# Kernel optimization log

Measured on AMD Instinct MI355X. Metric: run time of the kernel, lower is better.

The kernel has to match this reference:

```python
import jax, jax.numpy as jnp
import numpy as np


def sign_fn(x):
    # torch.sign(torch.sign(x) + 0.5): maps x >= 0 -> +1, x < 0 -> -1 (zero -> +1)
    return jnp.where(x >= 0, 1.0, -1.0).astype(x.dtype)


def setup_inputs() -> dict:
    key = jax.random.key(0)
    kx, kw, kb = jax.random.split(key, 3)
    TOKENS, IN, OUT = 8192, 4096, 4096
    x = jax.random.normal(kx, (TOKENS, IN), dtype=jnp.float32)
    weight = jax.random.normal(kw, (OUT, IN), dtype=jnp.float32)
    bias = jax.random.normal(kb, (OUT,), dtype=jnp.float32)
    return {"x": x, "weight": weight, "bias": bias}


def reference(x, weight, bias):
    b_weight = sign_fn(weight)  # [out, in], values in {+1, -1}
    b_bias = sign_fn(bias)      # [out]
    # nn.functional.linear: y = x @ W^T + b
    return jnp.einsum('ti,oi->to', x, b_weight) + b_bias
```

## Files before the change

### kernel.cpp

```cpp
#include <hip/hip_runtime.h>


typedef __attribute__((ext_vector_type(4))) int   i32x4;
typedef __attribute__((ext_vector_type(8))) short short8;
typedef __attribute__((ext_vector_type(4))) float f32x4;

constexpr int M = 8192;
constexpr int N = 4096;
constexpr int K = 4096;

constexpr int BM = 256, BN = 256, BK = 64;
constexpr int NTILES = K / BK;
constexpr int TILE_A = BM * BK;
constexpr int TILE_B = BN * BK;
constexpr int BUFSZ  = TILE_A + TILE_B;
constexpr int RING   = 4;

__device__ __forceinline__ void load_lds16(const void* g, void* l) {
    __builtin_amdgcn_global_load_lds(
        (const __attribute__((address_space(1))) unsigned int*)g,
        (__attribute__((address_space(3))) unsigned int*)l, 16, 0, 0);
}

constexpr int XB = M / 4;
constexpr int WB = 1024;
constexpr int WCH = N * K / 8;

__global__ __launch_bounds__(256) void prep_fused(
    const float* __restrict__ X, const float* __restrict__ W,
    signed char* __restrict__ Xq, signed char* __restrict__ Wq,
    float* __restrict__ Scale) {
    const int t    = threadIdx.x;
    const int lane = t & 63;
    const int wv   = t >> 6;

    if (blockIdx.x < XB) {
        const int row = blockIdx.x * 4 + wv;
        const float4* xr = reinterpret_cast<const float4*>(X + (size_t)row * K);
        float4 v[16];
        float mx = 0.f;
#pragma unroll
        for (int i = 0; i < 4; ++i) {
#pragma unroll
            for (int j = 0; j < 4; ++j) {
                float4 f = xr[4 * lane + 256 * i + j];
                v[4 * i + j] = f;
                mx = fmaxf(mx, fmaxf(fmaxf(fabsf(f.x), fabsf(f.y)),
                                     fmaxf(fabsf(f.z), fabsf(f.w))));
            }
        }
#pragma unroll
        for (int off = 32; off > 0; off >>= 1)
            mx = fmaxf(mx, __shfl_down(mx, off));
        mx = __shfl(mx, 0);
        const float rmax = fmaxf(mx, 1e-20f);
        const float inv  = 127.f / rmax;
        if (lane == 0) Scale[row] = rmax * (1.f / 127.f);

        uint4* out4 = reinterpret_cast<uint4*>(Xq + (size_t)row * K);
#pragma unroll
        for (int i = 0; i < 4; ++i) {
            uint4 o;
            unsigned int* op = &o.x;
#pragma unroll
            for (int j = 0; j < 4; ++j) {
                float4 f = v[4 * i + j];
                int q0 = (int)rintf(f.x * inv);
                int q1 = (int)rintf(f.y * inv);
                int q2 = (int)rintf(f.z * inv);
                int q3 = (int)rintf(f.w * inv);
                op[j] = (q0 & 255) | ((q1 & 255) << 8) |
                        ((q2 & 255) << 16) | ((unsigned)(q3 & 255) << 24);
            }
            out4[lane + 64 * i] = o;
        }
    } else {
        const float4* W4 = reinterpret_cast<const float4*>(W);
        uint2* O = reinterpret_cast<uint2*>(Wq);
        auto sg = [](float f) -> unsigned int { return (f >= 0.f) ? 1u : 0xFFu; };
        size_t idx = (size_t)(blockIdx.x - XB) * 256 + t;
        const size_t stride = (size_t)WB * 256;
        for (size_t c = idx; c < (size_t)WCH; c += stride) {
            float4 a = W4[c * 2], b = W4[c * 2 + 1];
            uint2 o;
            o.x = sg(a.x) | (sg(a.y) << 8) | (sg(a.z) << 16) | (sg(a.w) << 24);
            o.y = sg(b.x) | (sg(b.y) << 8) | (sg(b.z) << 16) | (sg(b.w) << 24);
            O[c] = o;
        }
    }
}

struct GemmCtx {
    const signed char* gA0;
    const signed char* gA1;
    const signed char* gB0;
    const signed char* gB1;
    signed char* lbase;
    int wm, wn, rl, cq16;
};

template <int P, bool STAGE>
__device__ __forceinline__ void phase(
    const GemmCtx& c, const signed char* Ab, const signed char* Bb,
    signed char* dst, size_t ko,
    i32x4 (&a)[2], i32x4 (&b)[4], i32x4 (&acc)[8][4]) {
    if constexpr (P == 0) {
#pragma unroll
        for (int ni = 0; ni < 4; ++ni)
            b[ni] = *reinterpret_cast<const i32x4*>(
                Bb + (c.wn * 64 + ni * 16 + c.rl) * BK + c.cq16);
    }
    a[0] = *reinterpret_cast<const i32x4*>(
        Ab + (c.wm * 128 + (2 * P + 0) * 16 + c.rl) * BK + c.cq16);
    a[1] = *reinterpret_cast<const i32x4*>(
        Ab + (c.wm * 128 + (2 * P + 1) * 16 + c.rl) * BK + c.cq16);
    if constexpr (STAGE) {
        if constexpr (P == 0) load_lds16(c.gA0 + ko, dst);
        if constexpr (P == 1) load_lds16(c.gA1 + ko, dst + 8192);
        if constexpr (P == 2) load_lds16(c.gB0 + ko, dst + TILE_A);
        if constexpr (P == 3) load_lds16(c.gB1 + ko, dst + TILE_A + 8192);
    }
    asm volatile("" ::: "memory");
    __builtin_amdgcn_s_barrier();
    asm volatile("s_waitcnt lgkmcnt(0)" ::: "memory");
    __builtin_amdgcn_sched_barrier(0);
    __builtin_amdgcn_s_setprio(1);
#pragma unroll
    for (int j = 0; j < 2; ++j)
#pragma unroll
        for (int ni = 0; ni < 4; ++ni)
            acc[2 * P + j][ni] = __builtin_amdgcn_mfma_i32_16x16x64_i8(
                a[j], b[ni], acc[2 * P + j][ni], 0, 0, 0);
    __builtin_amdgcn_s_setprio(0);
    asm volatile("" ::: "memory");
    if constexpr (P < 3) __builtin_amdgcn_s_barrier();
}

template <bool STAGE, int VMEND>
__device__ __forceinline__ void kstep8(
    const GemmCtx& c, const signed char* smem, int t,
    i32x4 (&a)[2], i32x4 (&b)[4], i32x4 (&acc)[8][4]) {
    const signed char* Ab = smem + (t & (RING - 1)) * BUFSZ;
    const signed char* Bb = Ab + TILE_A;
    signed char* dst = c.lbase + ((t + 3) & (RING - 1)) * BUFSZ;
    const size_t ko = (size_t)(t + 3) * BK;

    phase<0, STAGE>(c, Ab, Bb, dst, ko, a, b, acc);
    phase<1, STAGE>(c, Ab, Bb, dst, ko, a, b, acc);
    phase<2, STAGE>(c, Ab, Bb, dst, ko, a, b, acc);
    phase<3, STAGE>(c, Ab, Bb, dst, ko, a, b, acc);
    if constexpr (VMEND >= 0) {
        asm volatile("s_waitcnt vmcnt(%0)" :: "i"(VMEND) : "memory");
        __builtin_amdgcn_s_barrier();
        asm volatile("" ::: "memory");
    }
}

__global__ __launch_bounds__(512, 2) void gemm_i8_p(
    const signed char* __restrict__ Aq, const signed char* __restrict__ Bq,
    const float* __restrict__ Scale, const float* __restrict__ Bias,
    float* __restrict__ OUT) {
    __shared__ signed char smem[RING * BUFSZ];

    const int tid  = threadIdx.x;
    const int lane = tid & 63;
    const int w    = tid >> 6;
    GemmCtx c;
    c.wm = w >> 2;
    c.wn = w & 3;
    c.rl = lane & 15;
    c.cq16 = (((lane >> 4) ^ ((c.rl >> 1) & 3)) << 4);

    const int wg  = blockIdx.x;
    const int lin = (wg & 7) * 64 + (wg >> 3);
    const int n0  = (lin & 15) * BN;
    const int m0  = (lin >> 4) * BM;

    const int srow = tid >> 2;
    const int cg   = ((tid & 3) ^ ((srow >> 1) & 3)) * 16;
    c.gA0 = Aq + (size_t)(m0 + srow)       * K + cg;
    c.gA1 = Aq + (size_t)(m0 + 128 + srow) * K + cg;
    c.gB0 = Bq + (size_t)(n0 + srow)       * K + cg;
    c.gB1 = Bq + (size_t)(n0 + 128 + srow) * K + cg;
    c.lbase = smem + w * 1024;

    auto stage_full = [&](int t) {
        signed char* d = c.lbase + (t & (RING - 1)) * BUFSZ;
        const size_t ko = (size_t)t * BK;
        load_lds16(c.gA0 + ko, d);
        load_lds16(c.gA1 + ko, d + 8192);
        load_lds16(c.gB0 + ko, d + TILE_A);
        load_lds16(c.gB1 + ko, d + TILE_A + 8192);
    };

    i32x4 acc[8][4];
#pragma unroll
    for (int mi = 0; mi < 8; ++mi)
#pragma unroll
        for (int ni = 0; ni < 4; ++ni)
            acc[mi][ni] = (i32x4){0, 0, 0, 0};
    i32x4 a[2], b[4];

    stage_full(0); stage_full(1); stage_full(2);
    asm volatile("s_waitcnt vmcnt(8)" ::: "memory");
    __builtin_amdgcn_s_barrier();
    asm volatile("" ::: "memory");

    int t = 0;
    for (; t < NTILES - 3; ++t)
        kstep8<true, 8>(c, smem, t, a, b, acc);
    kstep8<false, 4>(c, smem, t, a, b, acc); ++t;
    kstep8<false, 0>(c, smem, t, a, b, acc); ++t;
    kstep8<false, -1>(c, smem, t, a, b, acc);

#pragma unroll
    for (int ni = 0; ni < 4; ++ni) {
        const int gcol = n0 + c.wn * 64 + ni * 16 + c.rl;
        const float sb = (Bias[gcol] >= 0.f) ? 1.f : -1.f;
#pragma unroll
        for (int mi = 0; mi < 8; ++mi) {
            const int growb = m0 + c.wm * 128 + mi * 16 + (lane >> 4) * 4;
            const float4 sc = *reinterpret_cast<const float4*>(&Scale[growb]);
            OUT[(size_t)(growb + 0) * N + gcol] = (float)acc[mi][ni][0] * sc.x + sb;
            OUT[(size_t)(growb + 1) * N + gcol] = (float)acc[mi][ni][1] * sc.y + sb;
            OUT[(size_t)(growb + 2) * N + gcol] = (float)acc[mi][ni][2] * sc.z + sb;
            OUT[(size_t)(growb + 3) * N + gcol] = (float)acc[mi][ni][3] * sc.w + sb;
        }
    }
}

constexpr int MT   = 128;
constexpr int NTF  = 128;
constexpr int LDSS = 40;
constexpr int KTB  = 32;
__device__ __forceinline__ unsigned short f2b(float f) {
    unsigned int u = __builtin_bit_cast(unsigned int, f);
    u += 0x7FFFu + ((u >> 16) & 1u);
    return (unsigned short)(u >> 16);
}
__global__ __launch_bounds__(256) void binlin_fallback(
    const float* __restrict__ X, const float* __restrict__ W,
    const float* __restrict__ B, float* __restrict__ OUT) {
    __shared__ unsigned short As[MT][LDSS];
    __shared__ unsigned short Bs[NTF][LDSS];
    const int tid  = threadIdx.x;
    const int lane = tid & 63;
    const int wave = tid >> 6;
    const int wm   = wave >> 1;
    const int wn   = wave & 1;
    const int m0 = blockIdx.y * MT;
    const int n0 = blockIdx.x * NTF;
    const int rl = lane & 15;
    const int kq = (lane >> 4) * 8;
    f32x4 acc[4][4];
#pragma unroll
    for (int mi = 0; mi < 4; ++mi)
#pragma unroll
        for (int ni = 0; ni < 4; ++ni)
            acc[mi][ni] = (f32x4){0.f, 0.f, 0.f, 0.f};
    for (int k0 = 0; k0 < K; k0 += KTB) {
#pragma unroll
        for (int it = 0; it < 4; ++it) {
            int g = tid + it * 256, row = g >> 3, c4 = (g & 7) << 2;
            float4 v = *reinterpret_cast<const float4*>(&X[(size_t)(m0 + row) * K + k0 + c4]);
            ushort4 h;
            h.x = f2b(v.x); h.y = f2b(v.y); h.z = f2b(v.z); h.w = f2b(v.w);
            *reinterpret_cast<ushort4*>(&As[row][c4]) = h;
        }
#pragma unroll
        for (int it = 0; it < 4; ++it) {
            int g = tid + it * 256, row = g >> 3, c4 = (g & 7) << 2;
            float4 v = *reinterpret_cast<const float4*>(&W[(size_t)(n0 + row) * K + k0 + c4]);
            ushort4 h;
            h.x = (v.x >= 0.f) ? 0x3F80u : 0xBF80u;
            h.y = (v.y >= 0.f) ? 0x3F80u : 0xBF80u;
            h.z = (v.z >= 0.f) ? 0x3F80u : 0xBF80u;
            h.w = (v.w >= 0.f) ? 0x3F80u : 0xBF80u;
            *reinterpret_cast<ushort4*>(&Bs[row][c4]) = h;
        }
        __syncthreads();
        short8 a[4], b[4];
#pragma unroll
        for (int mi = 0; mi < 4; ++mi)
            a[mi] = *reinterpret_cast<const short8*>(&As[wm * 64 + mi * 16 + rl][kq]);
#pragma unroll
        for (int ni = 0; ni < 4; ++ni)
            b[ni] = *reinterpret_cast<const short8*>(&Bs[wn * 64 + ni * 16 + rl][kq]);
#pragma unroll
        for (int mi = 0; mi < 4; ++mi)
#pragma unroll
            for (int ni = 0; ni < 4; ++ni)
                acc[mi][ni] = __builtin_amdgcn_mfma_f32_16x16x32_bf16(
                    a[mi], b[ni], acc[mi][ni], 0, 0, 0);
        __syncthreads();
    }
#pragma unroll
    for (int ni = 0; ni < 4; ++ni) {
        int gcol = n0 + wn * 64 + ni * 16 + rl;
        float sb = (B[gcol] >= 0.f) ? 1.f : -1.f;
#pragma unroll
        for (int mi = 0; mi < 4; ++mi) {
            int growb = m0 + wm * 64 + mi * 16 + (lane >> 4) * 4;
#pragma unroll
            for (int r = 0; r < 4; ++r)
                OUT[(size_t)(growb + r) * N + gcol] = acc[mi][ni][r] + sb;
        }
    }
}

extern "C" void kernel_launch(void* const* d_in, const int* in_sizes, int n_in,
                              void* d_out, int out_size, void* d_ws, size_t ws_size,
                              hipStream_t stream) {
    const float* x  = (const float*)d_in[0];
    const float* w  = (const float*)d_in[1];
    const float* b  = (const float*)d_in[2];
    float* out      = (float*)d_out;

    const size_t need = (size_t)M * K + (size_t)N * K + (size_t)M * sizeof(float);
    if (ws_size >= need) {
        signed char* Xq = (signed char*)d_ws;
        signed char* Wq = Xq + (size_t)M * K;
        float* Scale    = (float*)(Wq + (size_t)N * K);

        prep_fused<<<dim3(XB + WB), dim3(256), 0, stream>>>(x, w, Xq, Wq, Scale);
        gemm_i8_p<<<dim3((M / BM) * (N / BN)), dim3(512), 0, stream>>>(
            Xq, Wq, Scale, b, out);
    } else {
        dim3 grid(N / NTF, M / MT);
        binlin_fallback<<<grid, dim3(256), 0, stream>>>(x, w, b, out);
    }
}
```

Baseline: 403.2 us.

## Restructure int8 GEMM k-step from four barrier phases into two halves

Each K tile now runs as two halves of sixteen MFMAs instead of four phases of eight. That cuts the per-tile barrier count from about four to two and drops the explicit lgkmcnt waits between LDS reads and MFMAs. The vmcnt wait and barrier move to the start of each step, and the tail steps get new wait counts. The cost is more registers for A fragments held at once, which can strain occupancy at 2 workgroups per CU. It also relies on compiler-inserted waits for LDS reads and on the barrier placement to keep the ring buffer free of overwrite hazards.

```diff
diff --git a/kernel.cpp b/kernel.cpp
--- a/kernel.cpp
+++ b/kernel.cpp
@@ -99,61 +99,61 @@
     int wm, wn, rl, cq16;
 };
 
-template <int P, bool STAGE>
-__device__ __forceinline__ void phase(
-    const GemmCtx& c, const signed char* Ab, const signed char* Bb,
-    signed char* dst, size_t ko,
-    i32x4 (&a)[2], i32x4 (&b)[4], i32x4 (&acc)[8][4]) {
-    if constexpr (P == 0) {
-#pragma unroll
-        for (int ni = 0; ni < 4; ++ni)
-            b[ni] = *reinterpret_cast<const i32x4*>(
-                Bb + (c.wn * 64 + ni * 16 + c.rl) * BK + c.cq16);
-    }
-    a[0] = *reinterpret_cast<const i32x4*>(
-        Ab + (c.wm * 128 + (2 * P + 0) * 16 + c.rl) * BK + c.cq16);
-    a[1] = *reinterpret_cast<const i32x4*>(
-        Ab + (c.wm * 128 + (2 * P + 1) * 16 + c.rl) * BK + c.cq16);
-    if constexpr (STAGE) {
-        if constexpr (P == 0) load_lds16(c.gA0 + ko, dst);
-        if constexpr (P == 1) load_lds16(c.gA1 + ko, dst + 8192);
-        if constexpr (P == 2) load_lds16(c.gB0 + ko, dst + TILE_A);
-        if constexpr (P == 3) load_lds16(c.gB1 + ko, dst + TILE_A + 8192);
-    }
-    asm volatile("" ::: "memory");
-    __builtin_amdgcn_s_barrier();
-    asm volatile("s_waitcnt lgkmcnt(0)" ::: "memory");
-    __builtin_amdgcn_sched_barrier(0);
-    __builtin_amdgcn_s_setprio(1);
-#pragma unroll
-    for (int j = 0; j < 2; ++j)
-#pragma unroll
-        for (int ni = 0; ni < 4; ++ni)
-            acc[2 * P + j][ni] = __builtin_amdgcn_mfma_i32_16x16x64_i8(
-                a[j], b[ni], acc[2 * P + j][ni], 0, 0, 0);
-    __builtin_amdgcn_s_setprio(0);
-    asm volatile("" ::: "memory");
-    if constexpr (P < 3) __builtin_amdgcn_s_barrier();
-}
-
 template <bool STAGE, int VMEND>
-__device__ __forceinline__ void kstep8(
+__device__ __forceinline__ void kstep2(
     const GemmCtx& c, const signed char* smem, int t,
-    i32x4 (&a)[2], i32x4 (&b)[4], i32x4 (&acc)[8][4]) {
+    i32x4 (&b)[4], i32x4 (&acc)[8][4]) {
     const signed char* Ab = smem + (t & (RING - 1)) * BUFSZ;
     const signed char* Bb = Ab + TILE_A;
     signed char* dst = c.lbase + ((t + 3) & (RING - 1)) * BUFSZ;
     const size_t ko = (size_t)(t + 3) * BK;
 
-    phase<0, STAGE>(c, Ab, Bb, dst, ko, a, b, acc);
-    phase<1, STAGE>(c, Ab, Bb, dst, ko, a, b, acc);
-    phase<2, STAGE>(c, Ab, Bb, dst, ko, a, b, acc);
-    phase<3, STAGE>(c, Ab, Bb, dst, ko, a, b, acc);
-    if constexpr (VMEND >= 0) {
+    if constexpr (VMEND >= 0)
         asm volatile("s_waitcnt vmcnt(%0)" :: "i"(VMEND) : "memory");
-        __builtin_amdgcn_s_barrier();
-        asm volatile("" ::: "memory");
-    }
+    __builtin_amdgcn_s_barrier();
+
+    i32x4 a0[4];
+#pragma unroll
+    for (int ni = 0; ni < 4; ++ni)
+        b[ni] = *reinterpret_cast<const i32x4*>(
+            Bb + (c.wn * 64 + ni * 16 + c.rl) * BK + c.cq16);
+#pragma unroll
+    for (int mi = 0; mi < 4; ++mi)
+        a0[mi] = *reinterpret_cast<const i32x4*>(
+            Ab + (c.wm * 128 + mi * 16 + c.rl) * BK + c.cq16);
+    if constexpr (STAGE) {
+        load_lds16(c.gA0 + ko, dst);
+        load_lds16(c.gA1 + ko, dst + 8192);
+    }
+    __builtin_amdgcn_s_setprio(1);
+#pragma unroll
+    for (int mi = 0; mi < 4; ++mi)
+#pragma unroll
+        for (int ni = 0; ni < 4; ++ni)
+            acc[mi][ni] = __builtin_amdgcn_mfma_i32_16x16x64_i8(
+                a0[mi], b[ni], acc[mi][ni], 0, 0, 0);
+    __builtin_amdgcn_s_setprio(0);
+
+    i32x4 a1[4];
+#pragma unroll
+    for (int mi = 0; mi < 4; ++mi)
+        a1[mi] = *reinterpret_cast<const i32x4*>(
+            Ab + (c.wm * 128 + (4 + mi) * 16 + c.rl) * BK + c.cq16);
+    if constexpr (STAGE) {
+        load_lds16(c.gB0 + ko, dst + TILE_A);
+        load_lds16(c.gB1 + ko, dst + TILE_A + 8192);
+    }
+    asm volatile("" ::: "memory");
+    __builtin_amdgcn_s_barrier();
+    __builtin_amdgcn_s_setprio(1);
+#pragma unroll
+    for (int mi = 0; mi < 4; ++mi)
+#pragma unroll
+        for (int ni = 0; ni < 4; ++ni)
+            acc[4 + mi][ni] = __builtin_amdgcn_mfma_i32_16x16x64_i8(
+                a1[mi], b[ni], acc[4 + mi][ni], 0, 0, 0);
+    __builtin_amdgcn_s_setprio(0);
+    asm volatile("" ::: "memory");
 }
 
 __global__ __launch_bounds__(512, 2) void gemm_i8_p(
@@ -199,19 +199,16 @@
 #pragma unroll
         for (int ni = 0; ni < 4; ++ni)
             acc[mi][ni] = (i32x4){0, 0, 0, 0};
-    i32x4 a[2], b[4];
+    i32x4 b[4];
 
     stage_full(0); stage_full(1); stage_full(2);
-    asm volatile("s_waitcnt vmcnt(8)" ::: "memory");
-    __builtin_amdgcn_s_barrier();
-    asm volatile("" ::: "memory");
 
     int t = 0;
     for (; t < NTILES - 3; ++t)
-        kstep8<true, 8>(c, smem, t, a, b, acc);
-    kstep8<false, 4>(c, smem, t, a, b, acc); ++t;
-    kstep8<false, 0>(c, smem, t, a, b, acc); ++t;
-    kstep8<false, -1>(c, smem, t, a, b, acc);
+        kstep2<true, 8>(c, smem, t, b, acc);
+    kstep2<false, 8>(c, smem, t, b, acc); ++t;
+    kstep2<false, 4>(c, smem, t, b, acc); ++t;
+    kstep2<false, 0>(c, smem, t, b, acc);
 
 #pragma unroll
     for (int ni = 0; ni < 4; ++ni) {
```

Measured after the change: 405.5 us. About the same (+0.6%).
